# Kernel tuning notes

Measured on AMD Instinct MI355X. Metric: run time of the kernel, lower is better.

Reference implementation:

```python
import jax, jax.numpy as jnp
import numpy as np

SCALE_BASE = 512.0
GAMMA = 0.96875

def xpos(x, downscale=False):
    # x: (B, L, d). XPOS = rotary embedding with exponential position-dependent scale.
    B, L, d = x.shape
    half = d // 2
    scale_vec = (jnp.arange(0, d, 2, dtype=jnp.float32) + 0.4 * d) / (1.4 * d)  # (half,)
    pos = jnp.arange(L, dtype=jnp.float32)
    scale = scale_vec[None, :] ** (pos[:, None] / SCALE_BASE)  # (L, half)
    if downscale:
        scale = 1.0 / scale
    inv_freq = 1.0 / (10000.0 ** (jnp.arange(half, dtype=jnp.float32) / half))
    sinusoid = pos[:, None] * inv_freq[None, :]  # (L, half)
    sin_s = jnp.repeat(jnp.sin(sinusoid) * scale, 2, axis=-1)  # duplicate_interleave -> (L, d)
    cos_s = jnp.repeat(jnp.cos(sinusoid) * scale, 2, axis=-1)
    x1, x2 = x[..., ::2], x[..., 1::2]
    rot = jnp.stack((-x2, x1), axis=-1).reshape(x.shape)  # rotate_every_two
    return x * cos_s + rot * sin_s

def decay_mask(L, gamma):
    n = jnp.arange(L)[:, None]
    m = jnp.arange(L)[None, :]
    diff = n - m
    expo = jnp.where(diff >= 0, diff, 0).astype(jnp.float32)
    return jnp.where(diff >= 0, gamma ** expo, 0.0)  # (L, L) causal decay

def setup_inputs() -> dict:
    key = jax.random.key(0)
    kx, kq, kk, kv = jax.random.split(key, 4)
    B, L, H = 4, 2048, 1024
    hs = 1024  # head_size == v_dim
    X = jax.random.normal(kx, (B, L, H), dtype=jnp.float32)
    W_Q = jax.random.normal(kq, (H, hs), dtype=jnp.float32) / H
    W_K = jax.random.normal(kk, (H, hs), dtype=jnp.float32) / H
    W_V = jax.random.normal(kv, (H, hs), dtype=jnp.float32) / H
    return {"X": X, "W_Q": W_Q, "W_K": W_K, "W_V": W_V}

def reference(X, W_Q, W_K, W_V):
    L = X.shape[1]
    Q = xpos(X @ W_Q)
    K = xpos(X @ W_K, downscale=True)
    V = X @ W_V
    D = decay_mask(L, GAMMA)
    ret = jnp.einsum('bnd,bmd->bnm', Q, K) * D[None]  # (B, L, L)
    return ret @ V
```

## Files before the change

### kernel.cpp

```cpp
#include <hip/hip_runtime.h>
#include <cmath>

typedef __attribute__((ext_vector_type(8))) short short8;
typedef __attribute__((ext_vector_type(4))) short short4v;
typedef __attribute__((ext_vector_type(16))) float floatx16;
typedef unsigned short ushort_t;

#define LSEQ   2048
#define DMODEL 1024
#define BM 128
#define BN 128
#define BK 64
#define TPAD 136

#define L2GAMMA (-0.045803595f)
#define L2E4_512 (0.0259525632f)

__device__ __forceinline__ ushort_t f2b(float x) {
    union { float f; unsigned u; } v; v.f = x;
    unsigned r = v.u + 0x7fffu + ((v.u >> 16) & 1u);
    return (ushort_t)(r >> 16);
}

#define GLOAD_LDS16(gptr, lptr)                                                     \
    __builtin_amdgcn_global_load_lds(                                               \
        (const __attribute__((address_space(1))) unsigned int*)(gptr),              \
        (__attribute__((address_space(3))) unsigned int*)(lptr), 16, 0, 0)

__device__ __forceinline__ void gemm_core(
    const ushort_t* __restrict__ Ag, int lda, int aRow0,
    const ushort_t* __restrict__ Bg, int ldb, int bRow0,
    int kDepth, ushort_t* As, ushort_t* Bs, floatx16 acc[2][2])
{
    const int tid  = threadIdx.x;
    const int wave = tid >> 6, lane = tid & 63;
    const int wm = wave >> 1, wn = wave & 1;
    const int l31 = lane & 31, half = lane >> 5;
    const int srow = lane >> 3;
    const int scol = ((lane & 7) ^ srow) * 8;

    const ushort_t* ap[4];
    const ushort_t* bp[4];
    #pragma unroll
    for (int L = 0; L < 4; ++L) {
        int r = (wave * 4 + L) * 8 + srow;
        ap[L] = Ag + (size_t)(aRow0 + r) * lda + scol;
        bp[L] = Bg + (size_t)(bRow0 + r) * ldb + scol;
    }
    const int ldst = (lane >> 3) * BK + (lane & 7) * 8;

    for (int k0 = 0; k0 < kDepth; k0 += BK) {
        __syncthreads();
        #pragma unroll
        for (int L = 0; L < 4; ++L) {
            GLOAD_LDS16(ap[L], As + (wave * 4 + L) * (8 * BK) + ldst);
            GLOAD_LDS16(bp[L], Bs + (wave * 4 + L) * (8 * BK) + ldst);
            ap[L] += BK; bp[L] += BK;
        }
        __syncthreads();

        #pragma unroll
        for (int ks = 0; ks < 4; ++ks) {
            const int ch = ((ks * 2 + half) ^ (l31 & 7)) * 8;
            short8 a0 = *(const short8*)(As + (wm * 64      + l31) * BK + ch);
            short8 a1 = *(const short8*)(As + (wm * 64 + 32 + l31) * BK + ch);
            short8 b0 = *(const short8*)(Bs + (wn * 64      + l31) * BK + ch);
            short8 b1 = *(const short8*)(Bs + (wn * 64 + 32 + l31) * BK + ch);
            acc[0][0] = __builtin_amdgcn_mfma_f32_32x32x16_bf16(a0, b0, acc[0][0], 0, 0, 0);
            acc[0][1] = __builtin_amdgcn_mfma_f32_32x32x16_bf16(a0, b1, acc[0][1], 0, 0, 0);
            acc[1][0] = __builtin_amdgcn_mfma_f32_32x32x16_bf16(a1, b0, acc[1][0], 0, 0, 0);
            acc[1][1] = __builtin_amdgcn_mfma_f32_32x32x16_bf16(a1, b1, acc[1][1], 0, 0, 0);
        }
    }
}

__global__ __launch_bounds__(256) void xpos_table_kernel(float2* __restrict__ T)
{
    int idx = blockIdx.x * 256 + threadIdx.x;
    int l = idx & 2047;
    int p = (idx >> 11) & 511;
    int mode = idx >> 20;
    float sv = (2.0f * (float)p + 409.6f) * (1.0f / 1433.6f);
    float coeff = log2f(sv) * (1.0f / 512.0f) + L2GAMMA;
    float invf = exp2f(-(float)p * L2E4_512);
    float lf = (float)l;
    float s, c;
    sincosf(lf * invf, &s, &c);
    float g = exp2f((mode == 0 ? lf : -lf) * coeff);
    T[idx] = make_float2(c * g, s * g);
}

__global__ __launch_bounds__(256) void cast_x_kernel(
    const float4* __restrict__ X, short4v* __restrict__ Xb, int n4)
{
    int i = blockIdx.x * 256 + threadIdx.x;
    if (i < n4) {
        float4 v = X[i];
        short4v o;
        o.x = (short)f2b(v.x); o.y = (short)f2b(v.y);
        o.z = (short)f2b(v.z); o.w = (short)f2b(v.w);
        Xb[i] = o;
    }
}

__global__ __launch_bounds__(256) void wtrans_kernel(
    const float* __restrict__ Wq, const float* __restrict__ Wk,
    const float* __restrict__ Wv, ushort_t* __restrict__ Wt)
{
    const float* W = blockIdx.z == 0 ? Wq : blockIdx.z == 1 ? Wk : Wv;
    ushort_t* O = Wt + (size_t)blockIdx.z * (DMODEL * DMODEL);
    __shared__ float t[32][33];
    const int x = threadIdx.x & 31, y = (threadIdx.x >> 5) * 4;
    const int k0 = blockIdx.y * 32, n0 = blockIdx.x * 32;
    #pragma unroll
    for (int j = 0; j < 4; ++j)
        t[y + j][x] = W[(size_t)(k0 + y + j) * DMODEL + n0 + x];
    __syncthreads();
    #pragma unroll
    for (int j = 0; j < 4; ++j)
        O[(size_t)(n0 + y + j) * DMODEL + k0 + x] = f2b(t[x][y + j]);
}

__global__ __launch_bounds__(256, 4) void qkv_kernel(
    const ushort_t* __restrict__ Xb, const ushort_t* __restrict__ Wt,
    const float2* __restrict__ Tab,
    ushort_t* __restrict__ Q, ushort_t* __restrict__ Ko, ushort_t* __restrict__ Vt)
{
    __shared__ ushort_t smem[128 * TPAD];
    ushort_t* As = smem;
    ushort_t* Bs = smem + BM * BK;

    const int lin = blockIdx.x;
    const int inner = lin & 63;
    const int sup = lin >> 6;
    const int c = (sup % 3) * 8 + (inner & 7);
    const int r = (sup / 3) * 8 + (inner >> 3);
    const int mode = c >> 3;
    const int c0 = (c & 7) * BN;
    const int row0 = r * BM;

    floatx16 acc[2][2] = {};
    gemm_core(Xb, DMODEL, row0,
              Wt + (size_t)mode * (DMODEL * DMODEL), DMODEL, c0,
              DMODEL, As, Bs, acc);

    const int wave = threadIdx.x >> 6, lane = threadIdx.x & 63;
    const int wm = wave >> 1, wn = wave & 1;
    const int l31 = lane & 31, half = lane >> 5;
    const int rBase = row0 + wm * 64 + 4 * half;
    const int cBase = c0 + wn * 64 + l31;

    if (mode == 2) {
        const int colL0 = wn * 64 + l31;
        const int rowL0 = wm * 64 + 4 * half;
        __syncthreads();
        #pragma unroll
        for (int mi = 0; mi < 2; ++mi)
            #pragma unroll
            for (int ni = 0; ni < 2; ++ni)
                #pragma unroll
                for (int rg = 0; rg < 4; ++rg) {
                    short4v pk;
                    pk.x = (short)f2b(acc[mi][ni][rg * 4 + 0]);
                    pk.y = (short)f2b(acc[mi][ni][rg * 4 + 1]);
                    pk.z = (short)f2b(acc[mi][ni][rg * 4 + 2]);
                    pk.w = (short)f2b(acc[mi][ni][rg * 4 + 3]);
                    *(short4v*)(smem + (colL0 + ni * 32) * TPAD
                                     + rowL0 + mi * 32 + 8 * rg) = pk;
                }
        __syncthreads();
        const int t = threadIdx.x;
        const int colV = c0 + (t >> 1);
        const int lhalf = (t & 1) * 64;
        const int b = row0 >> 11, lpos0 = (row0 & 2047) + lhalf;
        #pragma unroll
        for (int i = 0; i < 8; ++i) {
            short8 vv = *(const short8*)(smem + (t >> 1) * TPAD + lhalf + i * 8);
            *(short8*)(Vt + (size_t)b * (LSEQ * DMODEL)
                          + (size_t)colV * LSEQ + lpos0 + i * 8) = vv;
        }
    } else {
        ushort_t* O = (mode == 0) ? Q : Ko;
        const float2* Tm = Tab + (size_t)mode * (512 * 2048);
        #pragma unroll
        for (int ni = 0; ni < 2; ++ni) {
            int col = cBase + ni * 32;
            const float2* tp = Tm + ((size_t)(col >> 1) << 11);
            #pragma unroll
            for (int mi = 0; mi < 2; ++mi)
                #pragma unroll
                for (int rg = 0; rg < 4; ++rg) {
                    int l0 = (rBase + mi * 32 + 8 * rg) & 2047;
                    float4 t01 = *(const float4*)(tp + l0);
                    float4 t23 = *(const float4*)(tp + l0 + 2);
                    float cs[8] = {t01.x, t01.y, t01.z, t01.w,
                                   t23.x, t23.y, t23.z, t23.w};
                    #pragma unroll
                    for (int q = 0; q < 4; ++q) {
                        int row = rBase + mi * 32 + 8 * rg + q;
                        float cc = cs[2 * q], ss = cs[2 * q + 1];
                        float v  = acc[mi][ni][rg * 4 + q];
                        float pv = __shfl_xor(v, 1);
                        float res = (lane & 1) ? fmaf(v, cc, pv * ss)
                                               : fmaf(v, cc, -pv * ss);
                        O[(size_t)row * DMODEL + col] = f2b(res);
                    }
                }
        }
    }
}

__global__ __launch_bounds__(256, 4) void score_kernel(
    const ushort_t* __restrict__ Q, const ushort_t* __restrict__ Kc,
    ushort_t* __restrict__ S)
{
    const int t = blockIdx.x, z = blockIdx.z;
    int bi, bj;
    if (t < 3) { bi = (t > 0); bj = t - (t > 0); }
    else { int u = t - 3; bi = 2 + u / 3; bj = bi - 2 + u % 3; }

    __shared__ ushort_t As[BM * BK], Bs[BN * BK];
    floatx16 acc[2][2] = {};
    const size_t zoff = (size_t)z * (LSEQ * DMODEL);
    gemm_core(Q + zoff, DMODEL, bi * BM, Kc + zoff, DMODEL, bj * BN,
              DMODEL, As, Bs, acc);

    const int wave = threadIdx.x >> 6, lane = threadIdx.x & 63;
    const int wm = wave >> 1, wn = wave & 1;
    const int l31 = lane & 31, half = lane >> 5;
    const int nBase = bi * BM + wm * 64 + 4 * half;
    const int mBase = bj * BN + wn * 64 + l31;
    ushort_t* Sz = S + (size_t)z * LSEQ * LSEQ;
    #pragma unroll
    for (int mi = 0; mi < 2; ++mi)
        #pragma unroll
        for (int ni = 0; ni < 2; ++ni) {
            int m = mBase + ni * 32;
            #pragma unroll
            for (int rg = 0; rg < 4; ++rg)
                #pragma unroll
                for (int q = 0; q < 4; ++q) {
                    int n = nBase + mi * 32 + 8 * rg + q;
                    Sz[(size_t)n * LSEQ + m] =
                        (m <= n) ? f2b(acc[mi][ni][rg * 4 + q]) : (ushort_t)0;
                }
        }
}

__global__ __launch_bounds__(256, 4) void av_kernel(
    const ushort_t* __restrict__ S, const ushort_t* __restrict__ Vt,
    float* __restrict__ Out)
{
    const int bx = blockIdx.x, bi = blockIdx.y, z = blockIdx.z;
    const int kLo = (bi >= 2) ? (bi - 2) * BM : 0;
    const int kW  = (bi + 1) * BM - kLo;
    __shared__ ushort_t As[BM * BK], Bs[BN * BK];
    floatx16 acc[2][2] = {};
    gemm_core(S + (size_t)z * LSEQ * LSEQ + kLo, LSEQ, bi * BM,
              Vt + (size_t)z * (LSEQ * DMODEL) + kLo, LSEQ, bx * BN,
              kW, As, Bs, acc);

    const int wave = threadIdx.x >> 6, lane = threadIdx.x & 63;
    const int wm = wave >> 1, wn = wave & 1;
    const int l31 = lane & 31, half = lane >> 5;
    const int rBase = bi * BM + wm * 64 + 4 * half;
    const int cBase = bx * BN + wn * 64 + l31;
    float* Oz = Out + (size_t)z * (LSEQ * DMODEL);
    #pragma unroll
    for (int mi = 0; mi < 2; ++mi)
        #pragma unroll
        for (int ni = 0; ni < 2; ++ni)
            #pragma unroll
            for (int rg = 0; rg < 4; ++rg)
                #pragma unroll
                for (int q = 0; q < 4; ++q)
                    Oz[(size_t)(rBase + mi * 32 + 8 * rg + q) * DMODEL
                       + cBase + ni * 32] = acc[mi][ni][rg * 4 + q];
}

extern "C" void kernel_launch(void* const* d_in, const int* in_sizes, int n_in,
                              void* d_out, int out_size, void* d_ws, size_t ws_size,
                              hipStream_t stream)
{
    const float* X  = (const float*)d_in[0];
    const float* Wq = (const float*)d_in[1];
    const float* Wk = (const float*)d_in[2];
    const float* Wv = (const float*)d_in[3];
    float* out = (float*)d_out;

    const size_t LH  = (size_t)LSEQ * DMODEL;
    const size_t WSZ = (size_t)DMODEL * DMODEL;
    const size_t SSZ = (size_t)LSEQ * LSEQ;
    const size_t TABN = (size_t)2 * 512 * 2048;

    size_t need4 = TABN * 8 + 2 * (3 * WSZ + 4 * (4 * LH + SSZ));
    const int bs = (ws_size >= need4) ? 4 : 1;

    float2* Tab = (float2*)d_ws;
    ushort_t* ws16 = (ushort_t*)(Tab + TABN);
    ushort_t* Wt = ws16;
    ushort_t* Xb = Wt + 3 * WSZ;
    ushort_t* Q  = Xb + (size_t)bs * LH;
    ushort_t* Kb = Q  + (size_t)bs * LH;
    ushort_t* Vt = Kb + (size_t)bs * LH;
    ushort_t* S  = Vt + (size_t)bs * LH;

    xpos_table_kernel<<<dim3(TABN / 256), 256, 0, stream>>>(Tab);
    wtrans_kernel<<<dim3(32, 32, 3), 256, 0, stream>>>(Wq, Wk, Wv, Wt);

    for (int p = 0; p < 4 / bs; ++p) {
        const float* Xp = X + (size_t)p * bs * LH;
        cast_x_kernel<<<dim3(bs * 2048), 256, 0, stream>>>(
            (const float4*)Xp, (short4v*)Xb, bs * (int)(LH / 4));
        qkv_kernel<<<dim3(24 * bs * 16), 256, 0, stream>>>(
            Xb, Wt, Tab, Q, Kb, Vt);
        score_kernel<<<dim3(45, 1, bs), 256, 0, stream>>>(Q, Kb, S);
        av_kernel<<<dim3(8, 16, bs), 256, 0, stream>>>(S, Vt,
            out + (size_t)p * bs * LH);
    }
}
```

Before: 224.4 us.

## Add 256x256-tile QKV projection kernel with 8-wave pipelined MFMA schedule

Adds a new QKV projection kernel that uses 256x256 output tiles, 512 threads and 128KB of dynamic LDS, replacing the 128-tile qkv_kernel when the shared-memory attribute can be set. Loads are double-buffered and interleaved with MFMA phases using barriers and setprio, and workgroups are remapped across XCDs for L2 locality. The V output is transposed through LDS for coalesced writes. The larger tiles raise arithmetic intensity and cut redundant global loads, at the cost of lower occupancy and a more complex synchronisation schedule.

```diff
diff --git a/kernel.cpp b/kernel.cpp
--- a/kernel.cpp
+++ b/kernel.cpp
@@ -210,6 +210,207 @@
     }
 }
 
+__global__ __launch_bounds__(512, 2) void qkv256_kernel(
+    const ushort_t* __restrict__ Xb, const ushort_t* __restrict__ Wt,
+    const float2* __restrict__ Tab,
+    ushort_t* __restrict__ Q, ushort_t* __restrict__ Ko, ushort_t* __restrict__ Vt)
+{
+    extern __shared__ ushort_t smem[];
+    const int tid  = threadIdx.x;
+    const int wave = tid >> 6, lane = tid & 63;
+    const int wm = wave >> 2, wn = wave & 3;
+    const int l31 = lane & 31, half = lane >> 5;
+    const int xl  = l31 & 7;
+
+    const int nwg = gridDim.x;
+    const int cpx = nwg >> 3;
+    const int orig = blockIdx.x;
+    const int wg = (orig & 7) * cpx + (orig >> 3);
+    const int sup = wg >> 4, inner = wg & 15;
+    const int ct = (sup % 3) * 4 + (inner & 3);
+    const int rt = (sup / 3) * 4 + (inner >> 2);
+    const int mode = ct >> 2;
+    const int row0 = rt << 8;
+    const int c0m  = (ct & 3) << 8;
+
+    const ushort_t* Bg = Wt + (size_t)mode * (DMODEL * DMODEL);
+
+    const int t8 = tid >> 3;
+    const int scol = (((tid & 7) ^ (t8 & 7)) << 3);
+    const ushort_t* Asrc = Xb + (size_t)(row0 + t8) * DMODEL + scol;
+    const ushort_t* Bsrc = Bg + (size_t)(c0m + t8) * DMODEL + scol;
+    char* ldsA = (char*)smem + tid * 16;
+    char* ldsB = (char*)smem + 65536 + tid * 16;
+
+#define STG_A(b, h, kt)                                                          \
+    do {                                                                         \
+        GLOAD_LDS16(Asrc + (size_t)((h) * 128) * DMODEL + (kt) * BK,             \
+                    ldsA + (b) * 32768 + (h) * 16384);                           \
+        GLOAD_LDS16(Asrc + (size_t)((h) * 128 + 64) * DMODEL + (kt) * BK,        \
+                    ldsA + (b) * 32768 + (h) * 16384 + 8192);                    \
+    } while (0)
+#define STG_B(b, h, kt)                                                          \
+    do {                                                                         \
+        GLOAD_LDS16(Bsrc + (size_t)((h) * 128) * DMODEL + (kt) * BK,             \
+                    ldsB + (b) * 32768 + (h) * 16384);                           \
+        GLOAD_LDS16(Bsrc + (size_t)((h) * 128 + 64) * DMODEL + (kt) * BK,        \
+                    ldsB + (b) * 32768 + (h) * 16384 + 8192);                    \
+    } while (0)
+
+#define MFMA8(accA, accB, af0, af1, bf)                                          \
+    do {                                                                         \
+        _Pragma("unroll")                                                        \
+        for (int ks = 0; ks < 4; ++ks) {                                         \
+            accA = __builtin_amdgcn_mfma_f32_32x32x16_bf16(af0[ks], bf[ks], accA, 0, 0, 0); \
+            accB = __builtin_amdgcn_mfma_f32_32x32x16_bf16(af1[ks], bf[ks], accB, 0, 0, 0); \
+        }                                                                        \
+    } while (0)
+
+    const int aBase = wm * 8192 + l31 * 64;
+    const int bBase = 32768 + (wn >> 1) * 8192 + ((wn & 1) * 64 + l31) * 64;
+
+    floatx16 acc[4][2] = {};
+    short8 a01[2][4], a23[2][4], b0f[4], b1f[4];
+
+    STG_A(0, 0, 0); STG_A(0, 1, 0); STG_B(0, 0, 0); STG_B(0, 1, 0);
+    STG_A(1, 0, 1);
+    asm volatile("s_waitcnt vmcnt(2)" ::: "memory");
+    __builtin_amdgcn_s_barrier();
+
+    #pragma unroll 2
+    for (int j = 0; j < 16; ++j) {
+        const int b = j & 1, nb = b ^ 1;
+        const int kt1 = (j + 1) & 15, kt2 = (j + 2) & 15;
+        const int ab = b * 16384 + aBase;
+        const int bb = b * 16384 + bBase;
+
+        #pragma unroll
+        for (int ks = 0; ks < 4; ++ks) {
+            const int ch = (((ks * 2 + half) ^ xl) << 3);
+            a01[0][ks] = *(const short8*)(smem + ab + ch);
+            a01[1][ks] = *(const short8*)(smem + ab + 2048 + ch);
+            b0f[ks]    = *(const short8*)(smem + bb + ch);
+        }
+        STG_A(nb, 1, kt1);
+        __builtin_amdgcn_s_barrier();
+        asm volatile("s_waitcnt lgkmcnt(0)" ::: "memory");
+        __builtin_amdgcn_sched_barrier(0);
+        __builtin_amdgcn_s_setprio(1);
+        MFMA8(acc[0][0], acc[1][0], a01[0], a01[1], b0f);
+        __builtin_amdgcn_s_setprio(0);
+        __builtin_amdgcn_s_barrier();
+
+        #pragma unroll
+        for (int ks = 0; ks < 4; ++ks) {
+            const int ch = (((ks * 2 + half) ^ xl) << 3);
+            b1f[ks] = *(const short8*)(smem + bb + 2048 + ch);
+        }
+        STG_B(nb, 0, kt1);
+        __builtin_amdgcn_s_barrier();
+        asm volatile("s_waitcnt lgkmcnt(0)" ::: "memory");
+        __builtin_amdgcn_sched_barrier(0);
+        __builtin_amdgcn_s_setprio(1);
+        MFMA8(acc[0][1], acc[1][1], a01[0], a01[1], b1f);
+        __builtin_amdgcn_s_setprio(0);
+        __builtin_amdgcn_s_barrier();
+
+        #pragma unroll
+        for (int ks = 0; ks < 4; ++ks) {
+            const int ch = (((ks * 2 + half) ^ xl) << 3);
+            a23[0][ks] = *(const short8*)(smem + ab + 2 * 2048 + ch);
+            a23[1][ks] = *(const short8*)(smem + ab + 3 * 2048 + ch);
+        }
+        STG_B(nb, 1, kt1);
+        __builtin_amdgcn_s_barrier();
+        asm volatile("s_waitcnt lgkmcnt(0)" ::: "memory");
+        __builtin_amdgcn_sched_barrier(0);
+        __builtin_amdgcn_s_setprio(1);
+        MFMA8(acc[2][0], acc[3][0], a23[0], a23[1], b0f);
+        __builtin_amdgcn_s_setprio(0);
+        __builtin_amdgcn_s_barrier();
+
+        STG_A(b, 0, kt2);
+        __builtin_amdgcn_s_barrier();
+        __builtin_amdgcn_s_setprio(1);
+        MFMA8(acc[2][1], acc[3][1], a23[0], a23[1], b1f);
+        __builtin_amdgcn_s_setprio(0);
+        asm volatile("s_waitcnt vmcnt(2)" ::: "memory");
+        __builtin_amdgcn_s_barrier();
+    }
+
+    const int rB = row0 + wm * 128 + 4 * half;
+    const int cB = c0m + wn * 64 + l31;
+
+    if (mode < 2) {
+        ushort_t* O = (mode == 0) ? Q : Ko;
+        const float2* Tm = Tab + (size_t)mode * (512 * 2048);
+        #pragma unroll
+        for (int n = 0; n < 2; ++n) {
+            const int col = cB + n * 32;
+            const float2* tp = Tm + ((size_t)(col >> 1) << 11);
+            #pragma unroll
+            for (int m = 0; m < 4; ++m)
+                #pragma unroll
+                for (int rg = 0; rg < 4; ++rg) {
+                    const int row = rB + m * 32 + 8 * rg;
+                    const int l0 = row & 2047;
+                    float4 t01 = *(const float4*)(tp + l0);
+                    float4 t23 = *(const float4*)(tp + l0 + 2);
+                    float cs[8] = {t01.x, t01.y, t01.z, t01.w,
+                                   t23.x, t23.y, t23.z, t23.w};
+                    #pragma unroll
+                    for (int q = 0; q < 4; ++q) {
+                        float v  = acc[m][n][rg * 4 + q];
+                        float pv = __shfl_xor(v, 1);
+                        float cc = cs[2 * q], ss = cs[2 * q + 1];
+                        float res = (lane & 1) ? fmaf(v, cc, pv * ss)
+                                               : fmaf(v, cc, -pv * ss);
+                        O[(size_t)(row + q) * DMODEL + col] = f2b(res);
+                    }
+                }
+        }
+    } else {
+        __syncthreads();
+        const int bidx = row0 >> 11, lpos0 = row0 & 2047;
+        #pragma unroll
+        for (int ph = 0; ph < 2; ++ph) {
+            if ((wn >> 1) == ph) {
+                const int colL = (wn & 1) * 64 + l31;
+                const int rowL = wm * 128 + 4 * half;
+                #pragma unroll
+                for (int m = 0; m < 4; ++m)
+                    #pragma unroll
+                    for (int n = 0; n < 2; ++n)
+                        #pragma unroll
+                        for (int rg = 0; rg < 4; ++rg) {
+                            short4v pk;
+                            pk.x = (short)f2b(acc[m][n][rg * 4 + 0]);
+                            pk.y = (short)f2b(acc[m][n][rg * 4 + 1]);
+                            pk.z = (short)f2b(acc[m][n][rg * 4 + 2]);
+                            pk.w = (short)f2b(acc[m][n][rg * 4 + 3]);
+                            *(short4v*)(smem + (size_t)(colL + n * 32) * 264
+                                             + rowL + m * 32 + 8 * rg) = pk;
+                        }
+            }
+            __syncthreads();
+            const int colV = c0m + ph * 128 + (tid >> 2);
+            const int qtr  = tid & 3;
+            #pragma unroll
+            for (int i = 0; i < 8; ++i) {
+                short8 vv = *(const short8*)(smem + (size_t)(tid >> 2) * 264
+                                                  + qtr * 64 + i * 8);
+                *(short8*)(Vt + (size_t)bidx * (LSEQ * DMODEL)
+                              + (size_t)colV * LSEQ + lpos0 + qtr * 64 + i * 8) = vv;
+            }
+            __syncthreads();
+        }
+    }
+    asm volatile("s_waitcnt vmcnt(0)" ::: "memory");
+#undef STG_A
+#undef STG_B
+#undef MFMA8
+}
+
 __global__ __launch_bounds__(256, 4) void score_kernel(
     const ushort_t* __restrict__ Q, const ushort_t* __restrict__ Kc,
     ushort_t* __restrict__ S)
@@ -305,6 +506,14 @@
     ushort_t* Vt = Kb + (size_t)bs * LH;
     ushort_t* S  = Vt + (size_t)bs * LH;
 
+    static int qkv256_ok = -1;
+    if (qkv256_ok < 0) {
+        hipError_t e = hipFuncSetAttribute(
+            reinterpret_cast<const void*>(qkv256_kernel),
+            hipFuncAttributeMaxDynamicSharedMemorySize, 131072);
+        qkv256_ok = (e == hipSuccess) ? 1 : 0;
+    }
+
     xpos_table_kernel<<<dim3(TABN / 256), 256, 0, stream>>>(Tab);
     wtrans_kernel<<<dim3(32, 32, 3), 256, 0, stream>>>(Wq, Wk, Wv, Wt);
 
@@ -312,8 +521,12 @@
         const float* Xp = X + (size_t)p * bs * LH;
         cast_x_kernel<<<dim3(bs * 2048), 256, 0, stream>>>(
             (const float4*)Xp, (short4v*)Xb, bs * (int)(LH / 4));
-        qkv_kernel<<<dim3(24 * bs * 16), 256, 0, stream>>>(
-            Xb, Wt, Tab, Q, Kb, Vt);
+        if (qkv256_ok)
+            qkv256_kernel<<<dim3(96 * bs), 512, 131072, stream>>>(
+                Xb, Wt, Tab, Q, Kb, Vt);
+        else
+            qkv_kernel<<<dim3(24 * bs * 16), 256, 0, stream>>>(
+                Xb, Wt, Tab, Q, Kb, Vt);
         score_kernel<<<dim3(45, 1, bs), 256, 0, stream>>>(Q, Kb, S);
         av_kernel<<<dim3(8, 16, bs), 256, 0, stream>>>(S, Vt,
             out + (size_t)p * bs * LH);
```

Measured after the change: 228.4 us. No clear change (+1.8%).

## Rewrite QKV projection with 16x16x32 MFMA tiles and XCD-aware block remap

Applied to the files above, without the earlier changes.

The QKV projection kernel now uses an inlined GEMM loop built on 16x16x32 bf16 MFMA instructions, with a 4x4 fragment grid per wave instead of 2x2 32x32 fragments. Block indices are remapped so consecutive blocks are spread across the 8 chiplets, which is meant to improve L2 reuse of X and weight tiles. The occupancy hint in launch_bounds is dropped and the epilogues are adapted to the new accumulator layout. Register pressure may rise and the remap assumes the grid size is a multiple of 8.

```diff
diff --git a/kernel.cpp b/kernel.cpp
--- a/kernel.cpp
+++ b/kernel.cpp
@@ -4,6 +4,7 @@
 typedef __attribute__((ext_vector_type(8))) short short8;
 typedef __attribute__((ext_vector_type(4))) short short4v;
 typedef __attribute__((ext_vector_type(16))) float floatx16;
+typedef __attribute__((ext_vector_type(4))) float float4v;
 typedef unsigned short ushort_t;
 
 #define LSEQ   2048
@@ -27,6 +28,9 @@
         (const __attribute__((address_space(1))) unsigned int*)(gptr),              \
         (__attribute__((address_space(3))) unsigned int*)(lptr), 16, 0, 0)
 
+#define MFMA_B16 __builtin_amdgcn_mfma_f32_32x32x16_bf16
+#define MFMA16   __builtin_amdgcn_mfma_f32_16x16x32_bf16
+
 __device__ __forceinline__ void gemm_core(
     const ushort_t* __restrict__ Ag, int lda, int aRow0,
     const ushort_t* __restrict__ Bg, int ldb, int bRow0,
@@ -66,10 +70,10 @@
             short8 a1 = *(const short8*)(As + (wm * 64 + 32 + l31) * BK + ch);
             short8 b0 = *(const short8*)(Bs + (wn * 64      + l31) * BK + ch);
             short8 b1 = *(const short8*)(Bs + (wn * 64 + 32 + l31) * BK + ch);
-            acc[0][0] = __builtin_amdgcn_mfma_f32_32x32x16_bf16(a0, b0, acc[0][0], 0, 0, 0);
-            acc[0][1] = __builtin_amdgcn_mfma_f32_32x32x16_bf16(a0, b1, acc[0][1], 0, 0, 0);
-            acc[1][0] = __builtin_amdgcn_mfma_f32_32x32x16_bf16(a1, b0, acc[1][0], 0, 0, 0);
-            acc[1][1] = __builtin_amdgcn_mfma_f32_32x32x16_bf16(a1, b1, acc[1][1], 0, 0, 0);
+            acc[0][0] = MFMA_B16(a0, b0, acc[0][0], 0, 0, 0);
+            acc[0][1] = MFMA_B16(a0, b1, acc[0][1], 0, 0, 0);
+            acc[1][0] = MFMA_B16(a1, b0, acc[1][0], 0, 0, 0);
+            acc[1][1] = MFMA_B16(a1, b1, acc[1][1], 0, 0, 0);
         }
     }
 }
@@ -121,7 +125,7 @@
         O[(size_t)(n0 + y + j) * DMODEL + k0 + x] = f2b(t[x][y + j]);
 }
 
-__global__ __launch_bounds__(256, 4) void qkv_kernel(
+__global__ __launch_bounds__(256) void qkv16_kernel(
     const ushort_t* __restrict__ Xb, const ushort_t* __restrict__ Wt,
     const float2* __restrict__ Tab,
     ushort_t* __restrict__ Q, ushort_t* __restrict__ Ko, ushort_t* __restrict__ Vt)
@@ -130,7 +134,9 @@
     ushort_t* As = smem;
     ushort_t* Bs = smem + BM * BK;
 
-    const int lin = blockIdx.x;
+    const int nwg = gridDim.x;
+    const int orig = blockIdx.x;
+    const int lin = (orig & 7) * (nwg >> 3) + (orig >> 3);
     const int inner = lin & 63;
     const int sup = lin >> 6;
     const int c = (sup % 3) * 8 + (inner & 7);
@@ -139,35 +145,103 @@
     const int c0 = (c & 7) * BN;
     const int row0 = r * BM;
 
-    floatx16 acc[2][2] = {};
-    gemm_core(Xb, DMODEL, row0,
-              Wt + (size_t)mode * (DMODEL * DMODEL), DMODEL, c0,
-              DMODEL, As, Bs, acc);
-
-    const int wave = threadIdx.x >> 6, lane = threadIdx.x & 63;
+    const int tid = threadIdx.x;
+    const int wave = tid >> 6, lane = tid & 63;
     const int wm = wave >> 1, wn = wave & 1;
-    const int l31 = lane & 31, half = lane >> 5;
-    const int rBase = row0 + wm * 64 + 4 * half;
-    const int cBase = c0 + wn * 64 + l31;
-
-    if (mode == 2) {
-        const int colL0 = wn * 64 + l31;
-        const int rowL0 = wm * 64 + 4 * half;
-        __syncthreads();
-        #pragma unroll
-        for (int mi = 0; mi < 2; ++mi)
-            #pragma unroll
-            for (int ni = 0; ni < 2; ++ni)
+    const int l15 = lane & 15, l4g = lane >> 4, l7 = lane & 7;
+
+    const int srow = lane >> 3;
+    const int scol = ((lane & 7) ^ srow) * 8;
+    const char* gA = (const char*)Xb;
+    const char* gB = (const char*)(Wt + (size_t)mode * (DMODEL * DMODEL));
+    unsigned aoff[4], boff[4];
+    #pragma unroll
+    for (int L = 0; L < 4; ++L) {
+        const int rr = (wave * 4 + L) * 8 + srow;
+        aoff[L] = (unsigned)(((row0 + rr) * DMODEL + scol) * 2);
+        boff[L] = (unsigned)(((c0 + rr) * DMODEL + scol) * 2);
+    }
+    const int ldst = srow * BK + (lane & 7) * 8;
+
+    int aBase[2], bBase[2];
+    #pragma unroll
+    for (int h = 0; h < 2; ++h) {
+        const int ch = ((h * 4 + l4g) ^ l7) * 8;
+        aBase[h] = (wm * 64 + l15) * BK + ch;
+        bBase[h] = (wn * 64 + l15) * BK + ch;
+    }
+
+    float4v acc[4][4] = {};
+
+    for (int k0 = 0; k0 < DMODEL; k0 += BK) {
+        __syncthreads();
+        #pragma unroll
+        for (int L = 0; L < 4; ++L) {
+            GLOAD_LDS16(gA + aoff[L], As + (wave * 4 + L) * (8 * BK) + ldst);
+            GLOAD_LDS16(gB + boff[L], Bs + (wave * 4 + L) * (8 * BK) + ldst);
+            aoff[L] += 2 * BK; boff[L] += 2 * BK;
+        }
+        __syncthreads();
+
+        #pragma unroll
+        for (int h = 0; h < 2; ++h) {
+            short8 a[4], b[4];
+            #pragma unroll
+            for (int f = 0; f < 4; ++f) {
+                a[f] = *(const short8*)(As + aBase[h] + f * (16 * BK));
+                b[f] = *(const short8*)(Bs + bBase[h] + f * (16 * BK));
+            }
+            #pragma unroll
+            for (int fr = 0; fr < 4; ++fr)
                 #pragma unroll
-                for (int rg = 0; rg < 4; ++rg) {
-                    short4v pk;
-                    pk.x = (short)f2b(acc[mi][ni][rg * 4 + 0]);
-                    pk.y = (short)f2b(acc[mi][ni][rg * 4 + 1]);
-                    pk.z = (short)f2b(acc[mi][ni][rg * 4 + 2]);
-                    pk.w = (short)f2b(acc[mi][ni][rg * 4 + 3]);
-                    *(short4v*)(smem + (colL0 + ni * 32) * TPAD
-                                     + rowL0 + mi * 32 + 8 * rg) = pk;
+                for (int fc = 0; fc < 4; ++fc)
+                    acc[fr][fc] = MFMA16(a[fr], b[fc], acc[fr][fc], 0, 0, 0);
+        }
+    }
+
+    const int rB = row0 + wm * 64 + l4g * 4;
+    const int cB = c0 + wn * 64 + l15;
+
+    if (mode < 2) {
+        ushort_t* O = (mode == 0) ? Q : Ko;
+        const float2* Tm = Tab + (size_t)mode * (512 * 2048);
+        #pragma unroll
+        for (int fc = 0; fc < 4; ++fc) {
+            const int col = cB + fc * 16;
+            const float2* tp = Tm + ((size_t)(col >> 1) << 11);
+            #pragma unroll
+            for (int fr = 0; fr < 4; ++fr) {
+                const int row = rB + fr * 16;
+                const int l0 = row & 2047;
+                float4 t01 = *(const float4*)(tp + l0);
+                float4 t23 = *(const float4*)(tp + l0 + 2);
+                float cs[8] = {t01.x, t01.y, t01.z, t01.w,
+                               t23.x, t23.y, t23.z, t23.w};
+                #pragma unroll
+                for (int q = 0; q < 4; ++q) {
+                    float v  = acc[fr][fc][q];
+                    float pv = __shfl_xor(v, 1);
+                    float cc = cs[2 * q], ss = cs[2 * q + 1];
+                    float res = (lane & 1) ? fmaf(v, cc, pv * ss)
+                                           : fmaf(v, cc, -pv * ss);
+                    O[(size_t)(row + q) * DMODEL + col] = f2b(res);
                 }
+            }
+        }
+    } else {
+        __syncthreads();
+        #pragma unroll
+        for (int fc = 0; fc < 4; ++fc)
+            #pragma unroll
+            for (int fr = 0; fr < 4; ++fr) {
+                short4v pk;
+                pk.x = (short)f2b(acc[fr][fc][0]);
+                pk.y = (short)f2b(acc[fr][fc][1]);
+                pk.z = (short)f2b(acc[fr][fc][2]);
+                pk.w = (short)f2b(acc[fr][fc][3]);
+                *(short4v*)(smem + (wn * 64 + fc * 16 + l15) * TPAD
+                                 + wm * 64 + fr * 16 + l4g * 4) = pk;
+            }
         __syncthreads();
         const int t = threadIdx.x;
         const int colV = c0 + (t >> 1);
@@ -178,34 +252,6 @@
             short8 vv = *(const short8*)(smem + (t >> 1) * TPAD + lhalf + i * 8);
             *(short8*)(Vt + (size_t)b * (LSEQ * DMODEL)
                           + (size_t)colV * LSEQ + lpos0 + i * 8) = vv;
-        }
-    } else {
-        ushort_t* O = (mode == 0) ? Q : Ko;
-        const float2* Tm = Tab + (size_t)mode * (512 * 2048);
-        #pragma unroll
-        for (int ni = 0; ni < 2; ++ni) {
-            int col = cBase + ni * 32;
-            const float2* tp = Tm + ((size_t)(col >> 1) << 11);
-            #pragma unroll
-            for (int mi = 0; mi < 2; ++mi)
-                #pragma unroll
-                for (int rg = 0; rg < 4; ++rg) {
-                    int l0 = (rBase + mi * 32 + 8 * rg) & 2047;
-                    float4 t01 = *(const float4*)(tp + l0);
-                    float4 t23 = *(const float4*)(tp + l0 + 2);
-                    float cs[8] = {t01.x, t01.y, t01.z, t01.w,
-                                   t23.x, t23.y, t23.z, t23.w};
-                    #pragma unroll
-                    for (int q = 0; q < 4; ++q) {
-                        int row = rBase + mi * 32 + 8 * rg + q;
-                        float cc = cs[2 * q], ss = cs[2 * q + 1];
-                        float v  = acc[mi][ni][rg * 4 + q];
-                        float pv = __shfl_xor(v, 1);
-                        float res = (lane & 1) ? fmaf(v, cc, pv * ss)
-                                               : fmaf(v, cc, -pv * ss);
-                        O[(size_t)row * DMODEL + col] = f2b(res);
-                    }
-                }
         }
     }
 }
@@ -312,7 +358,7 @@
         const float* Xp = X + (size_t)p * bs * LH;
         cast_x_kernel<<<dim3(bs * 2048), 256, 0, stream>>>(
             (const float4*)Xp, (short4v*)Xb, bs * (int)(LH / 4));
-        qkv_kernel<<<dim3(24 * bs * 16), 256, 0, stream>>>(
+        qkv16_kernel<<<dim3(24 * bs * 16), 256, 0, stream>>>(
             Xb, Wt, Tab, Q, Kb, Vt);
         score_kernel<<<dim3(45, 1, bs), 256, 0, stream>>>(Q, Kb, S);
         av_kernel<<<dim3(8, 16, bs), 256, 0, stream>>>(S, Vt,
```

Measured after the change: 213.2 us. 5.0% less time.
